# Performance work log

Measured on AMD Instinct MI355X. Metric: run time of the kernel, lower is better.

Reference implementation:

```python
import jax, jax.numpy as jnp
import numpy as np

B, S, IN_F, OUT_F = 4, 2048, 4096, 4096

def setup_inputs() -> dict:
    key = jax.random.key(0)
    k1, k2, k3 = jax.random.split(key, 3)
    # int8 activations and weights (symmetric range)
    x = jax.random.randint(k1, (B, S, IN_F), -128, 128, dtype=jnp.int32).astype(jnp.int8)
    weight_q = jax.random.randint(k2, (OUT_F, IN_F), -128, 128, dtype=jnp.int32).astype(jnp.int8)
    scale_x = jnp.float32(0.05)   # activation quant scale
    scale_w = jnp.float32(0.02)   # weight quant scale (scalar, per-tensor)
    scale_y = jax.random.uniform(k3, (OUT_F,), minval=0.5, maxval=2.0, dtype=jnp.float32)  # per-output-row scale
    return {"x": x, "weight_q": weight_q, "scale_x": scale_x, "scale_w": scale_w, "scale_y": scale_y}

def reference(x, weight_q, scale_x, scale_w, scale_y):
    # int8 GEMM with int32 accumulation: [B,S,IN] @ [OUT,IN]^T -> [B,S,OUT]
    acc = jax.lax.dot_general(x, weight_q, ((((2,), (1,)), ((), ()))),
                              preferred_element_type=jnp.int32)
    # fused requantization scale: scale_x * scale_w / scale_y  -> [OUT]
    requant_scale = (scale_x * scale_w / scale_y).astype(jnp.float32)
    out_f = acc.astype(jnp.float32) * requant_scale  # broadcast over last dim
    out_q = jnp.clip(jnp.round(out_f), -128, 127).astype(jnp.int8)
    return out_q, scale_y
```

## Files before the change

### kernel.cpp

```cpp
#include <hip/hip_runtime.h>
#include <cstdint>


#define MDIM 8192
#define NDIM 4096
#define KDIM 4096
#define BM 256
#define BN 256
#define BKB 64
#define NT (KDIM / BKB)

typedef int v4i __attribute__((ext_vector_type(4)));

#define FENCE() asm volatile("" ::: "memory")
#define BAR()                         \
  do {                                \
    FENCE();                          \
    __builtin_amdgcn_s_barrier();     \
    FENCE();                          \
  } while (0)

__device__ __forceinline__ uint32_t pack4(int a, int b, int c, int d) {
  return (uint32_t)(a & 0xFF) | ((uint32_t)(b & 0xFF) << 8) |
         ((uint32_t)(c & 0xFF) << 16) | ((uint32_t)(d & 0xFF) << 24);
}

__global__ __launch_bounds__(256) void pack_kernel(
    const int* __restrict__ x32, const int* __restrict__ w32,
    const float* __restrict__ sy, uint8_t* __restrict__ x8,
    uint8_t* __restrict__ w8, float* __restrict__ tail) {
  size_t idx = (size_t)blockIdx.x * blockDim.x + threadIdx.x;
  if (idx < (size_t)NDIM) tail[idx] = sy[idx];
  const size_t NX = (size_t)MDIM * KDIM;
  const size_t NW = (size_t)NDIM * KDIM;
  size_t base = idx * 16;
  const int* src;
  uint8_t* dst;
  if (base < NX) {
    src = x32 + base;
    dst = x8 + base;
  } else if (base < NX + NW) {
    src = w32 + (base - NX);
    dst = w8 + (base - NX);
  } else {
    return;
  }
  v4i a0 = *(const v4i*)(src + 0);
  v4i a1 = *(const v4i*)(src + 4);
  v4i a2 = *(const v4i*)(src + 8);
  v4i a3 = *(const v4i*)(src + 12);
  v4i o;
  o[0] = (int)pack4(a0[0], a0[1], a0[2], a0[3]);
  o[1] = (int)pack4(a1[0], a1[1], a1[2], a1[3]);
  o[2] = (int)pack4(a2[0], a2[1], a2[2], a2[3]);
  o[3] = (int)pack4(a3[0], a3[1], a3[2], a3[3]);
  *(v4i*)dst = o;
}

__global__ __launch_bounds__(512, 2) void gemm_kernel(
    const uint8_t* __restrict__ A8, const uint8_t* __restrict__ B8,
    const float* __restrict__ sxp, const float* __restrict__ swp,
    const float* __restrict__ syp, float* __restrict__ out) {
  __shared__ __align__(16) uint8_t lds[131072];

  const int tid = threadIdx.x;
  const int lane = tid & 63;
  const int wave = tid >> 6;

  const int nwg = (MDIM / BM) * (NDIM / BN);
  const int cpx = nwg / 8;
  const int wg = ((int)blockIdx.x % 8) * cpx + (int)blockIdx.x / 8;
  const int ntn = NDIM / BN;
  const int rowBase = (wg / ntn) * BM;
  const int colBase = (wg % ntn) * BN;

  const int wm2 = wave >> 2;
  const int wn4 = wave & 3;

  const int srow = wave * 16 + (lane >> 2);
  const int scol = (((lane & 3) ^ ((lane >> 2) & 3)) << 4);
  const uint32_t sdst = (uint32_t)(wave * 1024 + lane * 16);

  const int kl = lane >> 4;
  const int fr = lane & 15;
  const int swz = ((kl ^ (fr & 3)) << 4);

  uint32_t a_off[8], b_off[4];
#pragma unroll
  for (int i = 0; i < 8; i++)
    a_off[i] = (uint32_t)((wm2 * 128 + i * 16 + fr) * 64 + swz);
#pragma unroll
  for (int j = 0; j < 4; j++)
    b_off[j] = (uint32_t)(65536 + (wn4 * 64 + j * 16 + fr) * 64 + swz);

  v4i acc[8][4];
#pragma unroll
  for (int i = 0; i < 8; i++)
#pragma unroll
    for (int j = 0; j < 4; j++) acc[i][j] = (v4i){0, 0, 0, 0};

  auto stage = [&](int t) {
    const uint32_t ab = (uint32_t)(t & 3) * 16384u;
    const uint8_t* ga = A8 + (size_t)(rowBase + srow) * KDIM + t * BKB + scol;
    const uint8_t* gb = B8 + (size_t)(colBase + srow) * KDIM + t * BKB + scol;
    __builtin_amdgcn_global_load_lds(
        (const __attribute__((address_space(1))) void*)ga,
        (__attribute__((address_space(3))) void*)(lds + ab + sdst), 16, 0, 0);
    __builtin_amdgcn_global_load_lds(
        (const __attribute__((address_space(1))) void*)(ga + (size_t)128 * KDIM),
        (__attribute__((address_space(3))) void*)(lds + ab + 8192 + sdst), 16, 0, 0);
    __builtin_amdgcn_global_load_lds(
        (const __attribute__((address_space(1))) void*)gb,
        (__attribute__((address_space(3))) void*)(lds + 65536 + ab + sdst), 16, 0,
        0);
    __builtin_amdgcn_global_load_lds(
        (const __attribute__((address_space(1))) void*)(gb + (size_t)128 * KDIM),
        (__attribute__((address_space(3))) void*)(lds + 65536 + ab + 8192 + sdst),
        16, 0, 0);
  };

  stage(0);
  stage(1);

  for (int t = 0; t < NT; ++t) {
    if (t < NT - 1)
      asm volatile("s_waitcnt vmcnt(4)" ::: "memory");
    else
      asm volatile("s_waitcnt vmcnt(0)" ::: "memory");
    BAR();

    if (t + 2 < NT) stage(t + 2);

    const uint8_t* Ab = lds + (uint32_t)(t & 3) * 16384u;
    v4i af[8], bf[4];
#pragma unroll
    for (int i = 0; i < 8; i++) af[i] = *(const v4i*)(Ab + a_off[i]);
#pragma unroll
    for (int j = 0; j < 4; j++) bf[j] = *(const v4i*)(Ab + b_off[j]);
#pragma unroll
    for (int i = 0; i < 8; i++)
#pragma unroll
      for (int j = 0; j < 4; j++)
        acc[i][j] =
            __builtin_amdgcn_mfma_i32_16x16x64_i8(af[i], bf[j], acc[i][j], 0, 0, 0);
  }

  const float s = sxp[0] * swp[0];
  const int wrow = rowBase + wm2 * 128;
  const int wcol = colBase + wn4 * 64;
#pragma unroll
  for (int j = 0; j < 4; j++) {
    const int col = wcol + j * 16 + fr;
    const float rs = s / syp[col];
#pragma unroll
    for (int i = 0; i < 8; i++) {
      const int row0 = wrow + i * 16 + kl * 4;
#pragma unroll
      for (int r = 0; r < 4; r++) {
        float v = rintf((float)acc[i][j][r] * rs);
        v = fminf(127.f, fmaxf(-128.f, v));
        out[(size_t)(row0 + r) * NDIM + col] = v;
      }
    }
  }
}

extern "C" void kernel_launch(void* const* d_in, const int* in_sizes, int n_in,
                              void* d_out, int out_size, void* d_ws, size_t ws_size,
                              hipStream_t stream) {
  const int* x32 = (const int*)d_in[0];
  const int* w32 = (const int*)d_in[1];
  const float* sx = (const float*)d_in[2];
  const float* sw = (const float*)d_in[3];
  const float* sy = (const float*)d_in[4];
  float* out = (float*)d_out;
  float* tail = out + (size_t)MDIM * NDIM;

  uint8_t* x8 = (uint8_t*)d_ws;
  uint8_t* w8 = x8 + (size_t)MDIM * KDIM;
  const size_t need = (size_t)MDIM * KDIM + (size_t)NDIM * KDIM;
  (void)need;

  const int total16 = (int)(((size_t)MDIM * KDIM + (size_t)NDIM * KDIM) / 16);
  pack_kernel<<<(total16 + 255) / 256, 256, 0, stream>>>(x32, w32, sy, x8, w8,
                                                         tail);

  const int nblocks = (MDIM / BM) * (NDIM / BN);
  gemm_kernel<<<nblocks, 512, 0, stream>>>(x8, w8, sx, sw, sy, out);
}
```

Baseline: 195.0 us.

## Pre-swizzle operands into MFMA fragment order and use 128-wide K double buffering

The pack kernel now writes the int8 operands in a tiled layout that matches the MFMA fragment order, with 256-row by 128-K blocks stored contiguously. The GEMM can then stream each tile with linear global_load_lds copies and read fragments from LDS without swizzle arithmetic. The K tile grows from 64 to 128 and the pipeline changes from a 4-slot, prefetch-2 ring to a 2-slot double buffer. That double buffer needs an extra barrier per iteration, and the pack kernel's global reads become strided rather than linear.

Measured after the change: 182.2 us. 1.07x faster.

```diff
diff --git a/kernel.cpp b/kernel.cpp
--- a/kernel.cpp
+++ b/kernel.cpp
@@ -7,17 +7,18 @@
 #define KDIM 4096
 #define BM 256
 #define BN 256
-#define BKB 64
+#define BKB 128
 #define NT (KDIM / BKB)
+#define KTILES (KDIM / BKB)
 
 typedef int v4i __attribute__((ext_vector_type(4)));
 
 #define FENCE() asm volatile("" ::: "memory")
-#define BAR()                         \
-  do {                                \
-    FENCE();                          \
-    __builtin_amdgcn_s_barrier();     \
-    FENCE();                          \
+#define BAR()                     \
+  do {                            \
+    FENCE();                      \
+    __builtin_amdgcn_s_barrier(); \
+    FENCE();                      \
   } while (0)
 
 __device__ __forceinline__ uint32_t pack4(int a, int b, int c, int d) {
@@ -27,34 +28,46 @@
 
 __global__ __launch_bounds__(256) void pack_kernel(
     const int* __restrict__ x32, const int* __restrict__ w32,
-    const float* __restrict__ sy, uint8_t* __restrict__ x8,
-    uint8_t* __restrict__ w8, float* __restrict__ tail) {
-  size_t idx = (size_t)blockIdx.x * blockDim.x + threadIdx.x;
-  if (idx < (size_t)NDIM) tail[idx] = sy[idx];
-  const size_t NX = (size_t)MDIM * KDIM;
-  const size_t NW = (size_t)NDIM * KDIM;
-  size_t base = idx * 16;
+    const float* __restrict__ sy, uint8_t* __restrict__ x8f,
+    uint8_t* __restrict__ w8f, float* __restrict__ tail) {
+  const int t = blockIdx.x * 256 + threadIdx.x;
+  if (t < NDIM) tail[t] = sy[t];
+  const int NXC = (MDIM / 16) * KDIM;
+  const int NWC = (NDIM / 16) * KDIM;
+  if (t >= NXC + NWC) return;
   const int* src;
   uint8_t* dst;
-  if (base < NX) {
-    src = x32 + base;
-    dst = x8 + base;
-  } else if (base < NX + NW) {
-    src = w32 + (base - NX);
-    dst = w8 + (base - NX);
+  int chunk;
+  if (t < NXC) {
+    chunk = t;
+    src = x32;
+    dst = x8f;
   } else {
-    return;
+    chunk = t - NXC;
+    src = w32;
+    dst = w8f;
   }
-  v4i a0 = *(const v4i*)(src + 0);
-  v4i a1 = *(const v4i*)(src + 4);
-  v4i a2 = *(const v4i*)(src + 8);
-  v4i a3 = *(const v4i*)(src + 12);
+  const int blk = chunk >> 11;
+  const int cb = chunk & 2047;
+  const int mb = blk >> 5;
+  const int kt = blk & 31;
+  const int region = cb >> 6;
+  const int lpos = cb & 63;
+  const int rf = region >> 1, kh = region & 1;
+  const int kl = lpos >> 4, fr = lpos & 15;
+  const int r = mb * 256 + rf * 16 + fr;
+  const int k0 = kt * 128 + kh * 64 + kl * 16;
+  const int* s = src + (size_t)r * KDIM + k0;
+  v4i a0 = *(const v4i*)(s + 0);
+  v4i a1 = *(const v4i*)(s + 4);
+  v4i a2 = *(const v4i*)(s + 8);
+  v4i a3 = *(const v4i*)(s + 12);
   v4i o;
   o[0] = (int)pack4(a0[0], a0[1], a0[2], a0[3]);
   o[1] = (int)pack4(a1[0], a1[1], a1[2], a1[3]);
   o[2] = (int)pack4(a2[0], a2[1], a2[2], a2[3]);
   o[3] = (int)pack4(a3[0], a3[1], a3[2], a3[3]);
-  *(v4i*)dst = o;
+  *(v4i*)(dst + (size_t)chunk * 16) = o;
 }
 
 __global__ __launch_bounds__(512, 2) void gemm_kernel(
@@ -67,31 +80,15 @@
   const int lane = tid & 63;
   const int wave = tid >> 6;
 
-  const int nwg = (MDIM / BM) * (NDIM / BN);
-  const int cpx = nwg / 8;
-  const int wg = ((int)blockIdx.x % 8) * cpx + (int)blockIdx.x / 8;
-  const int ntn = NDIM / BN;
-  const int rowBase = (wg / ntn) * BM;
-  const int colBase = (wg % ntn) * BN;
+  const int wg = ((int)blockIdx.x % 8) * 64 + (int)blockIdx.x / 8;
+  const int mb = wg >> 4;
+  const int nb = wg & 15;
 
   const int wm2 = wave >> 2;
   const int wn4 = wave & 3;
 
-  const int srow = wave * 16 + (lane >> 2);
-  const int scol = (((lane & 3) ^ ((lane >> 2) & 3)) << 4);
-  const uint32_t sdst = (uint32_t)(wave * 1024 + lane * 16);
-
-  const int kl = lane >> 4;
-  const int fr = lane & 15;
-  const int swz = ((kl ^ (fr & 3)) << 4);
-
-  uint32_t a_off[8], b_off[4];
-#pragma unroll
-  for (int i = 0; i < 8; i++)
-    a_off[i] = (uint32_t)((wm2 * 128 + i * 16 + fr) * 64 + swz);
-#pragma unroll
-  for (int j = 0; j < 4; j++)
-    b_off[j] = (uint32_t)(65536 + (wn4 * 64 + j * 16 + fr) * 64 + swz);
+  const uint8_t* Abase = A8 + ((size_t)(mb * KTILES) << 15);
+  const uint8_t* Bbase = B8 + ((size_t)(nb * KTILES) << 15);
 
   v4i acc[8][4];
 #pragma unroll
@@ -99,55 +96,65 @@
 #pragma unroll
     for (int j = 0; j < 4; j++) acc[i][j] = (v4i){0, 0, 0, 0};
 
+  const uint32_t sdst = (uint32_t)tid * 16;
+
   auto stage = [&](int t) {
-    const uint32_t ab = (uint32_t)(t & 3) * 16384u;
-    const uint8_t* ga = A8 + (size_t)(rowBase + srow) * KDIM + t * BKB + scol;
-    const uint8_t* gb = B8 + (size_t)(colBase + srow) * KDIM + t * BKB + scol;
-    __builtin_amdgcn_global_load_lds(
-        (const __attribute__((address_space(1))) void*)ga,
-        (__attribute__((address_space(3))) void*)(lds + ab + sdst), 16, 0, 0);
-    __builtin_amdgcn_global_load_lds(
-        (const __attribute__((address_space(1))) void*)(ga + (size_t)128 * KDIM),
-        (__attribute__((address_space(3))) void*)(lds + ab + 8192 + sdst), 16, 0, 0);
-    __builtin_amdgcn_global_load_lds(
-        (const __attribute__((address_space(1))) void*)gb,
-        (__attribute__((address_space(3))) void*)(lds + 65536 + ab + sdst), 16, 0,
-        0);
-    __builtin_amdgcn_global_load_lds(
-        (const __attribute__((address_space(1))) void*)(gb + (size_t)128 * KDIM),
-        (__attribute__((address_space(3))) void*)(lds + 65536 + ab + 8192 + sdst),
-        16, 0, 0);
+    const uint32_t lb = (uint32_t)(t & 1) * 65536u;
+    const uint8_t* as = Abase + ((size_t)t << 15) + sdst;
+    const uint8_t* bs = Bbase + ((size_t)t << 15) + sdst;
+#pragma unroll
+    for (int r = 0; r < 4; ++r) {
+      __builtin_amdgcn_global_load_lds(
+          (const __attribute__((address_space(1))) void*)(as + r * 8192),
+          (__attribute__((address_space(3))) void*)(lds + lb + r * 8192 + sdst),
+          16, 0, 0);
+      __builtin_amdgcn_global_load_lds(
+          (const __attribute__((address_space(1))) void*)(bs + r * 8192),
+          (__attribute__((address_space(3))) void*)(lds + lb + 32768 + r * 8192 +
+                                                    sdst),
+          16, 0, 0);
+    }
   };
 
   stage(0);
-  stage(1);
 
   for (int t = 0; t < NT; ++t) {
-    if (t < NT - 1)
-      asm volatile("s_waitcnt vmcnt(4)" ::: "memory");
-    else
+    if (t + 1 < NT) {
+      stage(t + 1);
+      asm volatile("s_waitcnt vmcnt(8)" ::: "memory");
+    } else {
       asm volatile("s_waitcnt vmcnt(0)" ::: "memory");
+    }
     BAR();
 
-    if (t + 2 < NT) stage(t + 2);
-
-    const uint8_t* Ab = lds + (uint32_t)(t & 3) * 16384u;
-    v4i af[8], bf[4];
+    const uint8_t* La = lds + (uint32_t)(t & 1) * 65536u;
+    const uint8_t* Lb = La + 32768;
 #pragma unroll
-    for (int i = 0; i < 8; i++) af[i] = *(const v4i*)(Ab + a_off[i]);
+    for (int kh = 0; kh < 2; ++kh) {
+      v4i af[8], bf[4];
 #pragma unroll
-    for (int j = 0; j < 4; j++) bf[j] = *(const v4i*)(Ab + b_off[j]);
-#pragma unroll
-    for (int i = 0; i < 8; i++)
+      for (int i = 0; i < 8; i++)
+        af[i] = *(const v4i*)(La + ((((wm2 * 8 + i) << 1) + kh) << 10) +
+                              lane * 16);
 #pragma unroll
       for (int j = 0; j < 4; j++)
-        acc[i][j] =
-            __builtin_amdgcn_mfma_i32_16x16x64_i8(af[i], bf[j], acc[i][j], 0, 0, 0);
+        bf[j] = *(const v4i*)(Lb + ((((wn4 * 4 + j) << 1) + kh) << 10) +
+                              lane * 16);
+#pragma unroll
+      for (int i = 0; i < 8; i++)
+#pragma unroll
+        for (int j = 0; j < 4; j++)
+          acc[i][j] = __builtin_amdgcn_mfma_i32_16x16x64_i8(af[i], bf[j],
+                                                            acc[i][j], 0, 0, 0);
+    }
+    BAR();
   }
 
   const float s = sxp[0] * swp[0];
-  const int wrow = rowBase + wm2 * 128;
-  const int wcol = colBase + wn4 * 64;
+  const int kl = lane >> 4;
+  const int fr = lane & 15;
+  const int wrow = mb * 256 + wm2 * 128;
+  const int wcol = nb * 256 + wn4 * 64;
 #pragma unroll
   for (int j = 0; j < 4; j++) {
     const int col = wcol + j * 16 + fr;
@@ -176,15 +183,12 @@
   float* out = (float*)d_out;
   float* tail = out + (size_t)MDIM * NDIM;
 
-  uint8_t* x8 = (uint8_t*)d_ws;
-  uint8_t* w8 = x8 + (size_t)MDIM * KDIM;
-  const size_t need = (size_t)MDIM * KDIM + (size_t)NDIM * KDIM;
-  (void)need;
+  uint8_t* x8f = (uint8_t*)d_ws;
+  uint8_t* w8f = x8f + (size_t)MDIM * KDIM;
 
-  const int total16 = (int)(((size_t)MDIM * KDIM + (size_t)NDIM * KDIM) / 16);
-  pack_kernel<<<(total16 + 255) / 256, 256, 0, stream>>>(x32, w32, sy, x8, w8,
-                                                         tail);
+  const int total = (MDIM / 16) * KDIM + (NDIM / 16) * KDIM;
+  pack_kernel<<<total / 256, 256, 0, stream>>>(x32, w32, sy, x8f, w8f, tail);
 
   const int nblocks = (MDIM / BM) * (NDIM / BN);
-  gemm_kernel<<<nblocks, 512, 0, stream>>>(x8, w8, sx, sw, sy, out);
+  gemm_kernel<<<nblocks, 512, 0, stream>>>(x8f, w8f, sx, sw, sy, out);
 }
```
